# Kernel optimization log

Measured on AMD Instinct MI355X. Metric: run time of the kernel, lower is better.

## Reference

```python
import jax, jax.numpy as jnp
import numpy as np

B = 4194304  # batch of robot configurations
N_JOINTS = 6

# UR5-style DH parameters (match init config)
_A = np.array([0.0, -0.425, -0.3922, 0.0, 0.0, 0.0], dtype=np.float32)
_D = np.array([0.1625, 0.0, 0.0, 0.1333, 0.0997, 0.0996], dtype=np.float32)
_ALPHA = np.array([1.5708, 0.0, 0.0, 1.5708, -1.5708, 0.0], dtype=np.float32)


def setup_inputs() -> dict:
    key = jax.random.key(0)
    joint_angles = jax.random.normal(key, (B, N_JOINTS), dtype=jnp.float32)
    return {
        "joint_angles": joint_angles,
        "a": jnp.asarray(_A),
        "d": jnp.asarray(_D),
        "alpha": jnp.asarray(_ALPHA),
    }


def _fk(joint_angles, a, d, alpha):
    b, n = joint_angles.shape
    dt = joint_angles.dtype
    ct = jnp.cos(joint_angles)  # [B, n]
    st = jnp.sin(joint_angles)
    ca = jnp.cos(alpha)         # [n]
    sa = jnp.sin(alpha)
    zeros = jnp.zeros((b,), dt)
    ones = jnp.ones((b,), dt)
    cur = jnp.broadcast_to(jnp.eye(4, dtype=dt), (b, 4, 4))
    for i in range(n):  # fixed small joint count -> unrolled chain of 4x4 bmms
        cti, sti = ct[:, i], st[:, i]
        cai, sai, ai, di = ca[i], sa[i], a[i], d[i]
        T = jnp.stack([
            jnp.stack([cti, -sti * cai, sti * sai, ai * cti], axis=-1),
            jnp.stack([sti, cti * cai, -cti * sai, ai * sti], axis=-1),
            jnp.stack([zeros, zeros + sai, zeros + cai, zeros + di], axis=-1),
            jnp.stack([zeros, zeros, zeros, ones], axis=-1),
        ], axis=1)  # [B,4,4] DH transform for joint i
        cur = jnp.einsum('bij,bjk->bik', cur, T)
    return cur


def _matrix_to_quaternion(R):
    # Faithful to original: only the trace>0 branch is ever written; other
    # masks are computed but unused in the source, so q stays zero there.
    trace = R[:, 0, 0] + R[:, 1, 1] + R[:, 2, 2]
    mask = trace > 0
    trace_safe = jnp.where(mask, trace, 0.0)
    s = jnp.sqrt(trace_safe + 1.0) * 2.0
    s_safe = jnp.where(mask, s, 1.0)
    qw = jnp.where(mask, 0.25 * s, 0.0)
    qx = jnp.where(mask, (R[:, 2, 1] - R[:, 1, 2]) / s_safe, 0.0)
    qy = jnp.where(mask, (R[:, 0, 2] - R[:, 2, 0]) / s_safe, 0.0)
    qz = jnp.where(mask, (R[:, 1, 0] - R[:, 0, 1]) / s_safe, 0.0)
    return jnp.stack([qw, qx, qy, qz], axis=-1)


def reference(joint_angles, a, d, alpha):
    cur = _fk(joint_angles, a, d, alpha)          # [B,4,4] end-effector pose
    positions = cur[:, :3, 3]                      # [B,3]
    quats = _matrix_to_quaternion(cur[:, :3, :3])  # [B,4]
    return jnp.concatenate([positions, quats], axis=1)  # [B,7]
```

## Files before the change

### kernel.cpp

```cpp
#include <hip/hip_runtime.h>
#include <math.h>

#define B_TOTAL 4194304
#define NJ 6
#define BLK 256
#define RPT 4
#define ROWS (BLK * RPT)
#define OUT_F (ROWS * 7)

typedef float vf4 __attribute__((ext_vector_type(4)));

#define A1c (-0.425f)
#define A2c (-0.3922f)
#define D0c (0.1625f)
#define D3c (0.1333f)
#define D4c (0.0997f)
#define D5c (0.0996f)

__global__ void __launch_bounds__(BLK)
fk_kernel(const float* __restrict__ ja, const float* __restrict__ alpha,
          float* __restrict__ out) {
    __shared__ __align__(16) float s_out[OUT_F];

    const int t = threadIdx.x;
    const size_t blk = blockIdx.x;
    const float eps = cosf(alpha[0]);

    float flat[RPT * NJ];
    {
        const vf4* g4 = reinterpret_cast<const vf4*>(ja + (blk * ROWS + (size_t)t * RPT) * NJ);
#pragma unroll
        for (int k = 0; k < 6; ++k) {
            vf4 v = g4[k];
            flat[4 * k + 0] = v.x; flat[4 * k + 1] = v.y;
            flat[4 * k + 2] = v.z; flat[4 * k + 3] = v.w;
        }
    }

#pragma unroll
    for (int c = 0; c < RPT; ++c) {
        float sn[NJ], cs[NJ];
#pragma unroll
        for (int i = 0; i < NJ; ++i) __sincosf(flat[c * NJ + i], &sn[i], &cs[i]);

        float m00 = cs[0], m01 = -sn[0] * eps, m02 = sn[0],  m03 = 0.f;
        float m10 = sn[0], m11 =  cs[0] * eps, m12 = -cs[0], m13 = 0.f;
        float m20 = 0.f,   m21 = 1.f,          m22 = eps,    m23 = D0c;

#define ZROT_A(CT, ST, AA)                                          \
        { float u, v;                                               \
          u = m00 * CT + m01 * ST; v = m01 * CT - m00 * ST;         \
          m03 = AA * u + m03; m00 = u; m01 = v;                     \
          u = m10 * CT + m11 * ST; v = m11 * CT - m10 * ST;         \
          m13 = AA * u + m13; m10 = u; m11 = v;                     \
          u = m20 * CT + m21 * ST; v = m21 * CT - m20 * ST;         \
          m23 = AA * u + m23; m20 = u; m21 = v; }
        ZROT_A(cs[1], sn[1], A1c)
        ZROT_A(cs[2], sn[2], A2c)
#undef ZROT_A

        { float u, v;
          u = m00 * cs[3] + m01 * sn[3]; v = m01 * cs[3] - m00 * sn[3];
          m03 = D3c * m02 + m03; m00 = u; m01 = eps * v + m02; m02 = eps * m02 - v;
          u = m10 * cs[3] + m11 * sn[3]; v = m11 * cs[3] - m10 * sn[3];
          m13 = D3c * m12 + m13; m10 = u; m11 = eps * v + m12; m12 = eps * m12 - v;
          u = m20 * cs[3] + m21 * sn[3]; v = m21 * cs[3] - m20 * sn[3];
          m23 = D3c * m22 + m23; m20 = u; m21 = eps * v + m22; m22 = eps * m22 - v; }

        { float u, v;
          u = m00 * cs[4] + m01 * sn[4]; v = m01 * cs[4] - m00 * sn[4];
          m03 = D4c * m02 + m03; m00 = u; m01 = eps * v - m02; m02 = eps * m02 + v;
          u = m10 * cs[4] + m11 * sn[4]; v = m11 * cs[4] - m10 * sn[4];
          m13 = D4c * m12 + m13; m10 = u; m11 = eps * v - m12; m12 = eps * m12 + v;
          u = m20 * cs[4] + m21 * sn[4]; v = m21 * cs[4] - m20 * sn[4];
          m23 = D4c * m22 + m23; m20 = u; m21 = eps * v - m22; m22 = eps * m22 + v; }

        { float u, v;
          u = m00 * cs[5] + m01 * sn[5]; v = m01 * cs[5] - m00 * sn[5];
          m03 = D5c * m02 + m03; m00 = u; m01 = v;
          u = m10 * cs[5] + m11 * sn[5]; v = m11 * cs[5] - m10 * sn[5];
          m13 = D5c * m12 + m13; m10 = u; m11 = v;
          u = m20 * cs[5] + m21 * sn[5]; v = m21 * cs[5] - m20 * sn[5];
          m23 = D5c * m22 + m23; m20 = u; m21 = v; }

        float tr = m00 + m11 + m22;
        bool ok = tr > 0.f;
        float tr1 = tr + 1.f;
        float rr = __builtin_amdgcn_rsqf(ok ? tr1 : 1.f);
        float h = 0.5f * rr;

        float* p = s_out + ((size_t)t * RPT + c) * 7;
        p[0] = m03; p[1] = m13; p[2] = m23;
        p[3] = ok ? tr1 * h : 0.f;
        p[4] = ok ? (m21 - m12) * h : 0.f;
        p[5] = ok ? (m02 - m20) * h : 0.f;
        p[6] = ok ? (m10 - m01) * h : 0.f;
    }
    __syncthreads();

    {
        vf4* og4 = reinterpret_cast<vf4*>(out + blk * OUT_F);
        const vf4* ol4 = reinterpret_cast<const vf4*>(s_out);
#pragma unroll
        for (int k = 0; k < 7; ++k)
            __builtin_nontemporal_store(ol4[t + BLK * k], og4 + t + BLK * k);
    }
}

extern "C" void kernel_launch(void* const* d_in, const int* in_sizes, int n_in,
                              void* d_out, int out_size, void* d_ws, size_t ws_size,
                              hipStream_t stream) {
    const float* ja    = (const float*)d_in[0];
    const float* alpha = (const float*)d_in[3];
    float* out = (float*)d_out;
    int blocks = B_TOTAL / ROWS;
    fk_kernel<<<blocks, BLK, 0, stream>>>(ja, alpha, out);
}
```

Measured before the change: 37.38 us.

## Give each wavefront its own contiguous rows and drop the block barrier

Each wavefront now owns a contiguous 256-row slice. Lanes load rows with strided float2 reads, so each of the four per-thread rows sits 64 rows apart. Output is staged in a per-wave LDS region and written out by that wave alone, which lets the block-wide __syncthreads be removed. The change trades the earlier 16-byte contiguous per-thread loads for 8-byte loads and relies on intra-wave LDS ordering instead of an explicit barrier. The LDS write stride of 7 floats across lanes may also change bank conflict behaviour.

```diff
diff --git a/kernel.cpp b/kernel.cpp
--- a/kernel.cpp
+++ b/kernel.cpp
@@ -6,6 +6,7 @@
 #define BLK 256
 #define RPT 4
 #define ROWS (BLK * RPT)
+#define WAVE_ROWS 256
 #define OUT_F (ROWS * 7)
 
 typedef float vf4 __attribute__((ext_vector_type(4)));
@@ -23,25 +24,30 @@
     __shared__ __align__(16) float s_out[OUT_F];
 
     const int t = threadIdx.x;
+    const int lane = t & 63;
+    const int w = t >> 6;
     const size_t blk = blockIdx.x;
     const float eps = cosf(alpha[0]);
 
-    float flat[RPT * NJ];
-    {
-        const vf4* g4 = reinterpret_cast<const vf4*>(ja + (blk * ROWS + (size_t)t * RPT) * NJ);
+    const size_t rowBase = blk * ROWS + (size_t)w * WAVE_ROWS;
+
+    float th[RPT][NJ];
 #pragma unroll
-        for (int k = 0; k < 6; ++k) {
-            vf4 v = g4[k];
-            flat[4 * k + 0] = v.x; flat[4 * k + 1] = v.y;
-            flat[4 * k + 2] = v.z; flat[4 * k + 3] = v.w;
-        }
+    for (int c = 0; c < RPT; ++c) {
+        const float2* r2 = reinterpret_cast<const float2*>(ja + (rowBase + c * 64 + lane) * NJ);
+        float2 a0 = r2[0], a1 = r2[1], a2 = r2[2];
+        th[c][0] = a0.x; th[c][1] = a0.y;
+        th[c][2] = a1.x; th[c][3] = a1.y;
+        th[c][4] = a2.x; th[c][5] = a2.y;
     }
+
+    float* wbuf = s_out + (size_t)w * (WAVE_ROWS * 7);
 
 #pragma unroll
     for (int c = 0; c < RPT; ++c) {
         float sn[NJ], cs[NJ];
 #pragma unroll
-        for (int i = 0; i < NJ; ++i) __sincosf(flat[c * NJ + i], &sn[i], &cs[i]);
+        for (int i = 0; i < NJ; ++i) __sincosf(th[c][i], &sn[i], &cs[i]);
 
         float m00 = cs[0], m01 = -sn[0] * eps, m02 = sn[0],  m03 = 0.f;
         float m10 = sn[0], m11 =  cs[0] * eps, m12 = -cs[0], m13 = 0.f;
@@ -89,21 +95,20 @@
         float rr = __builtin_amdgcn_rsqf(ok ? tr1 : 1.f);
         float h = 0.5f * rr;
 
-        float* p = s_out + ((size_t)t * RPT + c) * 7;
+        float* p = wbuf + (c * 64 + lane) * 7;
         p[0] = m03; p[1] = m13; p[2] = m23;
         p[3] = ok ? tr1 * h : 0.f;
         p[4] = ok ? (m21 - m12) * h : 0.f;
         p[5] = ok ? (m02 - m20) * h : 0.f;
         p[6] = ok ? (m10 - m01) * h : 0.f;
     }
-    __syncthreads();
 
     {
-        vf4* og4 = reinterpret_cast<vf4*>(out + blk * OUT_F);
-        const vf4* ol4 = reinterpret_cast<const vf4*>(s_out);
+        vf4* og4 = reinterpret_cast<vf4*>(out + rowBase * 7);
+        const vf4* ol4 = reinterpret_cast<const vf4*>(wbuf);
 #pragma unroll
         for (int k = 0; k < 7; ++k)
-            __builtin_nontemporal_store(ol4[t + BLK * k], og4 + t + BLK * k);
+            __builtin_nontemporal_store(ol4[lane + 64 * k], og4 + lane + 64 * k);
     }
 }
 
```

Measured after the change: 38.28 us. 1.02x slower.
